# Optimization experiments

Measured on AMD Instinct MI355X. Metric: run time of the kernel, lower is better.

The kernel has to match this reference:

```python
import jax, jax.numpy as jnp
import numpy as np

B, S, D, H = 2, 2048, 1024, 16
HD = D // H  # head_dim = 64


def setup_inputs() -> dict:
    key = jax.random.key(0)
    ks = jax.random.split(key, 9)
    s_in = 1.0 / np.sqrt(D)
    inp = {
        "hidden_state": jax.random.normal(ks[0], (B, S, D), dtype=jnp.float32),
        # per-head projections, stacked: [H, D, HD]
        "Wq": jax.random.uniform(ks[1], (H, D, HD), jnp.float32, -s_in, s_in),
        "bq": jax.random.uniform(ks[2], (H, HD), jnp.float32, -s_in, s_in),
        "Wk": jax.random.uniform(ks[3], (H, D, HD), jnp.float32, -s_in, s_in),
        "bk": jax.random.uniform(ks[4], (H, HD), jnp.float32, -s_in, s_in),
        "Wv": jax.random.uniform(ks[5], (H, D, HD), jnp.float32, -s_in, s_in),
        "bv": jax.random.uniform(ks[6], (H, HD), jnp.float32, -s_in, s_in),
        # output linear: [D, D]
        "Wo": jax.random.uniform(ks[7], (D, D), jnp.float32, -s_in, s_in),
        "bo": jax.random.uniform(ks[8], (D,), jnp.float32, -s_in, s_in),
    }
    return inp


def reference(hidden_state, Wq, bq, Wk, bk, Wv, bv, Wo, bo):
    # fused per-head projections: [B, H, S, HD]
    q = jnp.einsum("bsd,hde->bhse", hidden_state, Wq) + bq[None, :, None, :]
    k = jnp.einsum("bsd,hde->bhse", hidden_state, Wk) + bk[None, :, None, :]
    v = jnp.einsum("bsd,hde->bhse", hidden_state, Wv) + bv[None, :, None, :]
    scale = 1.0 / jnp.sqrt(jnp.float32(HD))
    scores = jnp.einsum("bhse,bhte->bhst", q, k) * scale  # [B, H, S, S]
    weights = jax.nn.softmax(scores, axis=-1)
    ctx = jnp.einsum("bhst,bhte->bhse", weights, v)       # [B, H, S, HD]
    # concat heads along last dim -> [B, S, D]
    ctx = jnp.transpose(ctx, (0, 2, 1, 3)).reshape(B, S, D)
    return ctx @ Wo + bo
```

## Files before the change

kernel.cpp:

```cpp
#include <hip/hip_runtime.h>
#include <hip/hip_bf16.h>
#include <math.h>

#define BB 2
#define SS 2048
#define DD 1024
#define HH 16
#define HD 64

typedef __attribute__((ext_vector_type(8))) _Float16 f16x8;
typedef __attribute__((ext_vector_type(2))) __fp16 fp16x2;
typedef __attribute__((ext_vector_type(8))) unsigned short u16x8;
typedef __attribute__((ext_vector_type(4))) float f32x4;
typedef __attribute__((ext_vector_type(16))) float f32x16;
typedef __attribute__((ext_vector_type(4))) unsigned short u16x4;

__device__ __forceinline__ unsigned short hbits(_Float16 h) {
    union { _Float16 h; unsigned short s; } u; u.h = h; return u.s;
}

__device__ __forceinline__ int swz(int row, int grp) {
    return (row << 6) + (((grp) ^ (row & 7)) << 3);
}

__device__ __forceinline__ float fexp2(float x) {
#if __has_builtin(__builtin_amdgcn_exp2f)
    return __builtin_amdgcn_exp2f(x);
#else
    return exp2f(x);
#endif
}

__device__ __forceinline__ u16x4 pack4(float p0, float p1, float p2, float p3) {
#if __has_builtin(__builtin_amdgcn_cvt_pkrtz)
    union { fp16x2 h[2]; u16x4 u; } pu;
    pu.h[0] = __builtin_amdgcn_cvt_pkrtz(p0, p1);
    pu.h[1] = __builtin_amdgcn_cvt_pkrtz(p2, p3);
    return pu.u;
#else
    u16x4 r;
    r[0] = hbits((_Float16)p0); r[1] = hbits((_Float16)p1);
    r[2] = hbits((_Float16)p2); r[3] = hbits((_Float16)p3);
    return r;
#endif
}

__device__ __forceinline__ void gload_lds16(const unsigned short* g, unsigned short* l) {
#if __has_builtin(__builtin_amdgcn_global_load_lds)
    auto gp = (const __attribute__((address_space(1))) unsigned int*)(uintptr_t)g;
    auto lp = (__attribute__((address_space(3))) unsigned int*)(uintptr_t)l;
    __builtin_amdgcn_global_load_lds(gp, lp, 16, 0, 0);
#else
    *(u16x8*)(l + (threadIdx.x & 63) * 8) = *(const u16x8*)g;
#endif
}

__device__ __forceinline__ void wait4_barrier() {
    asm volatile("s_waitcnt vmcnt(4) lgkmcnt(0)\n\ts_barrier" ::: "memory");
}
__device__ __forceinline__ void wait6_barrier() {
    asm volatile("s_waitcnt vmcnt(6) lgkmcnt(0)\n\ts_barrier" ::: "memory");
}
__device__ __forceinline__ void wait0_barrier() {
    asm volatile("s_waitcnt vmcnt(0) lgkmcnt(0)\n\ts_barrier" ::: "memory");
}

__global__ __launch_bounds__(256) void prep_convert(
    const float* __restrict__ X,
    const float* __restrict__ Wq, const float* __restrict__ Wk,
    const float* __restrict__ Wv, const float* __restrict__ Wo,
    unsigned short* __restrict__ Xh2, unsigned short* __restrict__ WT)
{
    __shared__ __align__(16) unsigned short LT[64 * 68];
    const int bid = blockIdx.x;
    const int tid = threadIdx.x;

    if (bid < 2048) {
        const int mblk = bid >> 4;
        const int kg   = bid & 15;
        {
            const int r  = tid >> 3;
            const int c0 = (tid & 7) * 8;
            const float* src = X + (size_t)(mblk * 32 + r) * DD + kg * 64 + c0;
            float4 a = *(const float4*)src;
            float4 b = *(const float4*)(src + 4);
            unsigned short* d = &LT[r * 68 + c0];
            d[0] = hbits((_Float16)a.x); d[1] = hbits((_Float16)a.y);
            d[2] = hbits((_Float16)a.z); d[3] = hbits((_Float16)a.w);
            d[4] = hbits((_Float16)b.x); d[5] = hbits((_Float16)b.y);
            d[6] = hbits((_Float16)b.z); d[7] = hbits((_Float16)b.w);
        }
        __syncthreads();
        const int fbl = tid >> 6, l = tid & 63;
        const int row = l & 31, c = fbl * 16 + (l >> 5) * 8;
        u16x8 v = *(const u16x8*)&LT[row * 68 + c];
        *(u16x8*)&Xh2[((size_t)mblk * 64 + kg * 4 + fbl) * 512 + l * 8] = v;
        return;
    }

    const int t = bid - 2048;
    if (t < 768) {
        const int nt = t >> 4, ktile = t & 15;
        const int sel = nt >> 4, hh = nt & 15;
        const float* Ws = (sel == 0) ? Wq : ((sel == 1) ? Wk : Wv);
        const float* src = Ws + (size_t)hh * (DD * HD) + (size_t)ktile * 64 * HD;
        const int outRow0 = nt * 64;
        const int kcol0   = ktile * 64;

        const int e = tid & 63, dq = tid >> 6;
#pragma unroll
        for (int p = 0; p < 16; p++) {
            const int dl = p * 4 + dq;
            LT[e * 68 + dl] = hbits((_Float16)src[(size_t)dl * HD + e]);
        }
        __syncthreads();
#pragma unroll
        for (int p = 0; p < 2; p++) {
            const int sidx = p * 2048 + tid * 8;
            const int fb = sidx >> 9;
            const int l  = (sidx >> 3) & 63;
            const int nb = fb >> 2, kb = fb & 3;
            const int ee = nb * 32 + (l & 31);
            const int dl = kb * 16 + (l >> 5) * 8;
            u16x8 v = *(const u16x8*)&LT[ee * 68 + dl];
            *(u16x8*)&WT[(((size_t)(outRow0 >> 5) + nb) * 64 + (kcol0 >> 4) + kb) * 512
                         + l * 8] = v;
        }
    } else {
        const int tt = t - 768;
        const int nt = tt & 15, ktile = tt >> 4;
        const float* src = Wo + (size_t)ktile * 64 * DD + nt * 64;
        const int outRow0 = 3072 + nt * 64;
        const int kcol0 = ktile * 64;

        const int e = tid & 63, dq = tid >> 6;
#pragma unroll
        for (int p = 0; p < 16; p++) {
            const int dl = p * 4 + dq;
            LT[e * 68 + dl] = hbits((_Float16)src[(size_t)dl * DD + e]);
        }
        __syncthreads();
        const int eo = tid >> 2, d16 = (tid & 3) * 16;
#pragma unroll
        for (int j = 0; j < 4; j++) {
            *(ushort4*)&WT[(size_t)(outRow0 + eo) * DD + kcol0 + d16 + j * 4] =
                *(const ushort4*)&LT[eo * 68 + d16 + j * 4];
        }
    }
}

#define GBM 128
#define GBN 128
#define GBK 64
#define NKT (DD / GBK)
#define QBK 32
#define QNKT (DD / QBK)

__global__ __launch_bounds__(256, 3) void qkv_gemm(
    const unsigned short* __restrict__ Xh2, const unsigned short* __restrict__ WT2,
    const float* __restrict__ bq, const float* __restrict__ bk,
    const float* __restrict__ bv,
    unsigned short* __restrict__ qh, unsigned short* __restrict__ kh,
    unsigned short* __restrict__ vTs, unsigned int* __restrict__ kc2)
{
    __shared__ __align__(16) unsigned short As[3][8 * 512];
    __shared__ __align__(16) unsigned short Bs[3][8 * 512];

    const int tid  = threadIdx.x;
    const int m0   = blockIdx.y * GBM;
    const int n0   = blockIdx.x * GBN;
    const int lane = tid & 63;
    const int w    = tid >> 6;
    const int wm   = w & 1, wn = w >> 1;
    const int l31  = lane & 31, h = lane >> 5;

    f32x16 acc[2][2];
#pragma unroll
    for (int i = 0; i < 2; i++)
#pragma unroll
        for (int j = 0; j < 2; j++)
#pragma unroll
            for (int k = 0; k < 16; k++) acc[i][j][k] = 0.f;

    const size_t mb0 = (size_t)(m0 >> 5);
    const size_t nb0 = (size_t)(n0 >> 5);

    auto STAGE = [&](int buf, int t) {
#pragma unroll
        for (int p = 0; p < 4; p++) {
            const int c = p * 4 + w;
            const unsigned short* src;
            unsigned short* dst;
            if (c < 8) {
                src = Xh2 + ((mb0 + (c >> 1)) * 64 + t * 2 + (c & 1)) * 512 + lane * 8;
                dst = &As[buf][c * 512];
            } else {
                const int d = c - 8;
                src = WT2 + ((nb0 + (d >> 1)) * 64 + t * 2 + (d & 1)) * 512 + lane * 8;
                dst = &Bs[buf][d * 512];
            }
            gload_lds16(src, dst);
        }
    };

    STAGE(0, 0);
    STAGE(1, 1);
    wait0_barrier();

    int cur = 0, pre = 2;
    for (int t = 0; t < QNKT; t++) {
        if (t + 2 < QNKT) STAGE(pre, t + 2);
        f16x8 af[2][2], bf[2][2];
#pragma unroll
        for (int mi = 0; mi < 2; mi++)
#pragma unroll
            for (int kb = 0; kb < 2; kb++)
                af[mi][kb] = *(const f16x8*)
                    &As[cur][(((wm * 2 + mi) << 1) + kb) * 512 + lane * 8];
#pragma unroll
        for (int ni = 0; ni < 2; ni++)
#pragma unroll
            for (int kb = 0; kb < 2; kb++)
                bf[ni][kb] = *(const f16x8*)
                    &Bs[cur][(((wn * 2 + ni) << 1) + kb) * 512 + lane * 8];
#pragma unroll
        for (int kb = 0; kb < 2; kb++)
#pragma unroll
            for (int mi = 0; mi < 2; mi++)
#pragma unroll
                for (int ni = 0; ni < 2; ni++)
                    acc[mi][ni] = __builtin_amdgcn_mfma_f32_32x32x16_f16(
                        af[mi][kb], bf[ni][kb], acc[mi][ni], 0, 0, 0);
        if (t < QNKT - 2)       wait4_barrier();
        else if (t == QNKT - 2) wait0_barrier();
        cur = (cur == 2) ? 0 : cur + 1;
        pre = (pre == 2) ? 0 : pre + 1;
    }

    const int sel = n0 >> 10;
    const int hw  = ((n0 + wn * 64) >> 6) & 15;
    const int bblk = m0 >> 11;
    const float* bias = (sel == 0) ? bq : ((sel == 1) ? bk : bv);
    const size_t bh_base = ((size_t)bblk * HH + hw) * (size_t)SS * HD;
    float wmx = 0.0f;
#pragma unroll
    for (int mi = 0; mi < 2; mi++) {
#pragma unroll
        for (int r = 0; r < 16; r++) {
            const int srow = wm * 64 + mi * 32 + (r & 3) + 8 * (r >> 2) + 4 * h;
            const int s = (m0 + srow) & (SS - 1);
            const int s63 = s & 63;
            float v2 = 0.0f;
#pragma unroll
            for (int ni = 0; ni < 2; ni++) {
                const int e = ni * 32 + l31;
                const float val = acc[mi][ni][r] + bias[hw * HD + e];
                if (sel == 0) {
                    qh[bh_base + (size_t)s * HD + e] = hbits((_Float16)val);
                } else if (sel == 1) {
                    v2 = fmaf(val, val, v2);
                    kh[bh_base + (size_t)(s >> 6) * 4096 + swz(s63, e >> 3) + (e & 7)] =
                        hbits((_Float16)val);
                } else {
                    vTs[bh_base + (size_t)(s >> 6) * 4096 + swz(e, s63 >> 3) + (s63 & 7)] =
                        hbits((_Float16)val);
                }
            }
            if (sel == 1) {
                v2 += __shfl_xor(v2, 1);
                v2 += __shfl_xor(v2, 2);
                v2 += __shfl_xor(v2, 4);
                v2 += __shfl_xor(v2, 8);
                v2 += __shfl_xor(v2, 16);
                wmx = fmaxf(wmx, v2);
            }
        }
    }
    if (sel == 1) {
        wmx = fmaxf(wmx, __shfl_xor(wmx, 32));
        if (lane == 0)
            atomicMax(&kc2[bblk * HH + hw], __float_as_uint(wmx));
    }
}

__global__ __launch_bounds__(256, 2) void out_gemm(
    const unsigned short* __restrict__ Ctxh, const unsigned short* __restrict__ WoT,
    const float* __restrict__ bo, float* __restrict__ out)
{
    __shared__ __align__(16) unsigned short As[3][16 * 512];
    __shared__ __align__(16) unsigned short Bs[3][8 * 512];

    const int tid = threadIdx.x;
    const int f  = blockIdx.y * 16 + blockIdx.x;
    const int fs = (f & 7) * 64 + (f >> 3);
    const int bx = fs % 16, by = fs / 16;
    const int m0 = by * 128;
    const int n0 = bx * 64;
    const int lane = tid & 63;
    const int w = tid >> 6;
    const int wm = w & 1, wn = w >> 1;
    const int l15 = lane & 15, quad = lane >> 4;

    int g_off[4];
#pragma unroll
    for (int p = 0; p < 4; p++) {
        const int c = p * 4 + w;
        g_off[p] = ((c >> 1) * 16 + l15) * DD + (c & 1) * 32 + quad * 8;
    }

    f32x4 acc[4][2];
#pragma unroll
    for (int i = 0; i < 4; i++)
#pragma unroll
        for (int j = 0; j < 2; j++) acc[i][j] = (f32x4){0.f, 0.f, 0.f, 0.f};

    const unsigned short* Abase = Ctxh + (size_t)m0 * DD;
    const unsigned short* Bbase = WoT + (size_t)n0 * DD;

#pragma unroll
    for (int p = 0; p < 4; p++)
        gload_lds16(Abase + g_off[p], &As[0][(p * 4 + w) * 512]);
#pragma unroll
    for (int p = 0; p < 2; p++)
        gload_lds16(Bbase + g_off[p], &Bs[0][(p * 4 + w) * 512]);
#pragma unroll
    for (int p = 0; p < 4; p++)
        gload_lds16(Abase + g_off[p] + GBK, &As[1][(p * 4 + w) * 512]);
#pragma unroll
    for (int p = 0; p < 2; p++)
        gload_lds16(Bbase + g_off[p] + GBK, &Bs[1][(p * 4 + w) * 512]);
    wait0_barrier();

    int cur = 0, pre = 2;
    for (int it = 0; it < NKT; it++) {
        if (it + 2 < NKT) {
            const int kt2 = (it + 2) * GBK;
#pragma unroll
            for (int p = 0; p < 4; p++)
                gload_lds16(Abase + g_off[p] + kt2, &As[pre][(p * 4 + w) * 512]);
#pragma unroll
            for (int p = 0; p < 2; p++)
                gload_lds16(Bbase + g_off[p] + kt2, &Bs[pre][(p * 4 + w) * 512]);
        }
#pragma unroll
        for (int ks = 0; ks < 2; ks++) {
            f16x8 af[4], bf[2];
#pragma unroll
            for (int i = 0; i < 4; i++)
                af[i] = *(const f16x8*)&As[cur][((wm * 4 + i) * 2 + ks) * 512 + lane * 8];
#pragma unroll
            for (int j = 0; j < 2; j++)
                bf[j] = *(const f16x8*)&Bs[cur][((wn * 2 + j) * 2 + ks) * 512 + lane * 8];
#pragma unroll
            for (int ns = 0; ns < 2; ns++)
#pragma unroll
                for (int ms = 0; ms < 4; ms++)
                    acc[ms][ns] = __builtin_amdgcn_mfma_f32_16x16x32_f16(
                        af[ms], bf[ns], acc[ms][ns], 0, 0, 0);
        }
        if (it < NKT - 2)       wait6_barrier();
        else if (it == NKT - 2) wait0_barrier();
        cur = (cur == 2) ? 0 : cur + 1;
        pre = (pre == 2) ? 0 : pre + 1;
    }

#pragma unroll
    for (int ms = 0; ms < 4; ms++) {
#pragma unroll
        for (int rr = 0; rr < 4; rr++) {
            const size_t m = (size_t)(m0 + wm * 64 + ms * 16 + quad * 4 + rr);
#pragma unroll
            for (int ns = 0; ns < 2; ns++) {
                const int n = n0 + wn * 32 + ns * 16 + l15;
                out[m * DD + n] = acc[ms][ns][rr] + bo[n];
            }
        }
    }
}

#define TQB 128
#define TKB 64
#define NT (SS / TKB)
#define C1 0.1803368801111204f

__global__ __launch_bounds__(256, 2) void attn_mfma(
    const unsigned short* __restrict__ qh, const unsigned short* __restrict__ kh,
    const unsigned short* __restrict__ vTs, const unsigned int* __restrict__ kc2,
    unsigned short* __restrict__ ctxh)
{
    __shared__ __align__(16) unsigned short KL [3][TKB * 64];
    __shared__ __align__(16) unsigned short VtL[3][HD * 64];
    __shared__ __align__(16) unsigned short PsL[4][32 * 64];

    const int tid  = threadIdx.x;
    const int lane = tid & 63;
    const int w    = tid >> 6;
    const int l15  = lane & 15;
    const int quad = lane >> 4;
    const int f  = blockIdx.y * 16 + blockIdx.x;
    const int fs = (f & 7) * 64 + (f >> 3);
    const int bh = fs >> 4;
    const int q0 = (fs & 15) * TQB;

    const float kfac = sqrtf(__uint_as_float(kc2[bh])) * 1.01f * C1;

    f16x8 qf[2][2];
    float M2[2];
#pragma unroll
    for (int msub = 0; msub < 2; msub++) {
        const unsigned short* qrow =
            qh + ((size_t)bh * SS + q0 + w * 32 + msub * 16 + l15) * HD;
        float nq2 = 0.0f;
#pragma unroll
        for (int dstep = 0; dstep < 2; dstep++) {
            qf[msub][dstep] = *(const f16x8*)&qrow[dstep * 32 + quad * 8];
#pragma unroll
            for (int j = 0; j < 8; j++) {
                const float x = (float)qf[msub][dstep][j];
                nq2 = fmaf(x, x, nq2);
            }
        }
        nq2 += __shfl_xor(nq2, 16);
        nq2 += __shfl_xor(nq2, 32);
        M2[msub] = sqrtf(nq2) * kfac;
    }

    f16x8 ones;
#pragma unroll
    for (int j = 0; j < 8; j++) ones[j] = (_Float16)1.0f;

    f32x4 o[2][4], lones[2];
#pragma unroll
    for (int ms = 0; ms < 2; ms++) {
        lones[ms] = (f32x4){0.f, 0.f, 0.f, 0.f};
#pragma unroll
        for (int e = 0; e < 4; e++) o[ms][e] = (f32x4){0.f, 0.f, 0.f, 0.f};
    }

    const unsigned short* kb0 = kh  + (size_t)bh * SS * HD;
    const unsigned short* vb0 = vTs + (size_t)bh * SS * HD;

    gload_lds16(kb0 + tid * 8,        &KL [0][w * 512]);
    gload_lds16(kb0 + 2048 + tid * 8, &KL [0][2048 + w * 512]);
    gload_lds16(vb0 + tid * 8,        &VtL[0][w * 512]);
    gload_lds16(vb0 + 2048 + tid * 8, &VtL[0][2048 + w * 512]);
    gload_lds16(kb0 + 4096 + tid * 8, &KL [1][w * 512]);
    gload_lds16(kb0 + 6144 + tid * 8, &KL [1][2048 + w * 512]);
    gload_lds16(vb0 + 4096 + tid * 8, &VtL[1][w * 512]);
    gload_lds16(vb0 + 6144 + tid * 8, &VtL[1][2048 + w * 512]);
    wait0_barrier();

    int cur = 0, pre = 2;
    for (int t = 0; t < NT; t++) {
        if (t + 2 < NT) {
            const unsigned short* kb = kb0 + (size_t)(t + 2) * 4096;
            const unsigned short* vb = vb0 + (size_t)(t + 2) * 4096;
            gload_lds16(kb + tid * 8,        &KL [pre][w * 512]);
            gload_lds16(kb + 2048 + tid * 8, &KL [pre][2048 + w * 512]);
            gload_lds16(vb + tid * 8,        &VtL[pre][w * 512]);
            gload_lds16(vb + 2048 + tid * 8, &VtL[pre][2048 + w * 512]);
        }

        f32x4 sc[2][4];
        __builtin_amdgcn_s_setprio(1);
#pragma unroll
        for (int ksub = 0; ksub < 4; ksub++) {
            const int row = ksub * 16 + l15;
            f16x8 k0 = *(const f16x8*)&KL[cur][swz(row, quad)];
            f16x8 k1 = *(const f16x8*)&KL[cur][swz(row, 4 + quad)];
#pragma unroll
            for (int msub = 0; msub < 2; msub++) {
                f32x4 a = (f32x4){0.f, 0.f, 0.f, 0.f};
                a = __builtin_amdgcn_mfma_f32_16x16x32_f16(k0, qf[msub][0], a, 0, 0, 0);
                a = __builtin_amdgcn_mfma_f32_16x16x32_f16(k1, qf[msub][1], a, 0, 0, 0);
                sc[msub][ksub] = a;
            }
        }
        __builtin_amdgcn_s_setprio(0);

#pragma unroll
        for (int msub = 0; msub < 2; msub++) {
            const int prow = msub * 16 + l15;
#pragma unroll
            for (int ksub = 0; ksub < 4; ksub++) {
                const float p0 = fexp2(fmaf(sc[msub][ksub][0], C1, -M2[msub]));
                const float p1 = fexp2(fmaf(sc[msub][ksub][1], C1, -M2[msub]));
                const float p2 = fexp2(fmaf(sc[msub][ksub][2], C1, -M2[msub]));
                const float p3 = fexp2(fmaf(sc[msub][ksub][3], C1, -M2[msub]));
                *(u16x4*)&PsL[w][swz(prow, ksub * 2 + (quad >> 1)) + (quad & 1) * 4] =
                    pack4(p0, p1, p2, p3);
            }
        }

        __builtin_amdgcn_s_setprio(1);
#pragma unroll
        for (int kj = 0; kj < 2; kj++) {
            f16x8 pa[2];
#pragma unroll
            for (int msub = 0; msub < 2; msub++)
                pa[msub] = *(const f16x8*)&PsL[w][swz(msub * 16 + l15, kj * 4 + quad)];
            lones[0] = __builtin_amdgcn_mfma_f32_16x16x32_f16(pa[0], ones, lones[0], 0, 0, 0);
            lones[1] = __builtin_amdgcn_mfma_f32_16x16x32_f16(pa[1], ones, lones[1], 0, 0, 0);
#pragma unroll
            for (int esub = 0; esub < 4; esub++) {
                f16x8 vr = *(const f16x8*)&VtL[cur][swz(esub * 16 + l15, kj * 4 + quad)];
                o[0][esub] = __builtin_amdgcn_mfma_f32_16x16x32_f16(pa[0], vr, o[0][esub], 0, 0, 0);
                o[1][esub] = __builtin_amdgcn_mfma_f32_16x16x32_f16(pa[1], vr, o[1][esub], 0, 0, 0);
            }
        }
        __builtin_amdgcn_s_setprio(0);

        if (t < NT - 2)       wait4_barrier();
        else if (t == NT - 2) wait0_barrier();
        cur = (cur == 2) ? 0 : cur + 1;
        pre = (pre == 2) ? 0 : pre + 1;
    }

    const int b = bh >> 4;
    const int hh = bh & 15;
#pragma unroll
    for (int msub = 0; msub < 2; msub++) {
#pragma unroll
        for (int rr = 0; rr < 4; rr++) {
            const float linv = 1.0f / lones[msub][rr];
            const int row = q0 + w * 32 + msub * 16 + quad * 4 + rr;
#pragma unroll
            for (int esub = 0; esub < 4; esub++) {
                ctxh[((size_t)b * SS + row) * DD + hh * HD + esub * 16 + l15] =
                    hbits((_Float16)(o[msub][esub][rr] * linv));
            }
        }
    }
}

extern "C" void kernel_launch(void* const* d_in, const int* in_sizes, int n_in,
                              void* d_out, int out_size, void* d_ws, size_t ws_size,
                              hipStream_t stream) {
    const float* X  = (const float*)d_in[0];
    const float* Wq = (const float*)d_in[1];
    const float* bq = (const float*)d_in[2];
    const float* Wk = (const float*)d_in[3];
    const float* bk = (const float*)d_in[4];
    const float* Wv = (const float*)d_in[5];
    const float* bv = (const float*)d_in[6];
    const float* Wo = (const float*)d_in[7];
    const float* bo = (const float*)d_in[8];
    float* out = (float*)d_out;

    const size_t NB2 = (size_t)4096 * 1024 * 2;
    unsigned char* w8 = (unsigned char*)d_ws;
    unsigned short* Xh2  = (unsigned short*)(w8);
    unsigned short* WT   = (unsigned short*)(w8 + NB2);
    unsigned short* qh   = (unsigned short*)(w8 + 2 * NB2);
    unsigned short* kh   = (unsigned short*)(w8 + 3 * NB2);
    unsigned short* vTs  = (unsigned short*)(w8 + 4 * NB2);
    unsigned short* ctxh = (unsigned short*)(w8 + 5 * NB2);
    unsigned int*   kc2  = (unsigned int*)(w8 + 6 * NB2);
    unsigned short* WoT  = WT + (size_t)3072 * 1024;

    (void)hipMemsetAsync(kc2, 0, BB * HH * sizeof(unsigned int), stream);

    prep_convert<<<dim3(3072), 256, 0, stream>>>(X, Wq, Wk, Wv, Wo, Xh2, WT);

    qkv_gemm<<<dim3(3072 / GBN, 4096 / GBM), 256, 0, stream>>>(
        Xh2, WT, bq, bk, bv, qh, kh, vTs, kc2);

    attn_mfma<<<dim3(SS / TQB, BB * HH), 256, 0, stream>>>(qh, kh, vTs, kc2, ctxh);

    out_gemm<<<dim3(1024 / 64, 4096 / 128), 256, 0, stream>>>(ctxh, WoT, bo, out);
}
```

Measured before the change: 214.4 us.

## Switch attention to 32x32x16 MFMA tiles with per-lane row-sum accumulation

Rewrites the attention inner loop to use 32x32x16 f16 MFMAs, so each wave handles its 32 query rows as one tile, in place of 16x16x32 MFMAs over two 16-row subtiles. The score layout now gives each lane one query row, so the softmax denominator is summed directly in VALU instead of via an extra MFMA against a ones vector. The output is written as 4-element vector stores. This cuts MFMA instruction count and removes the ones-MFMA overhead, but changes register pressure and LDS access patterns, and the K/V tile is now processed in two 32-key halves.

```diff
diff --git a/kernel.cpp b/kernel.cpp
--- a/kernel.cpp
+++ b/kernel.cpp
@@ -395,8 +395,8 @@
     const int tid  = threadIdx.x;
     const int lane = tid & 63;
     const int w    = tid >> 6;
-    const int l15  = lane & 15;
-    const int quad = lane >> 4;
+    const int l31  = lane & 31;
+    const int h    = lane >> 5;
     const int f  = blockIdx.y * 16 + blockIdx.x;
     const int fs = (f & 7) * 64 + (f >> 3);
     const int bh = fs >> 4;
@@ -404,38 +404,31 @@
 
     const float kfac = sqrtf(__uint_as_float(kc2[bh])) * 1.01f * C1;
 
-    f16x8 qf[2][2];
-    float M2[2];
-#pragma unroll
-    for (int msub = 0; msub < 2; msub++) {
+    f16x8 qf[4];
+    float M2;
+    {
         const unsigned short* qrow =
-            qh + ((size_t)bh * SS + q0 + w * 32 + msub * 16 + l15) * HD;
+            qh + ((size_t)bh * SS + q0 + w * 32 + l31) * HD;
         float nq2 = 0.0f;
 #pragma unroll
-        for (int dstep = 0; dstep < 2; dstep++) {
-            qf[msub][dstep] = *(const f16x8*)&qrow[dstep * 32 + quad * 8];
+        for (int kf = 0; kf < 4; kf++) {
+            qf[kf] = *(const f16x8*)&qrow[kf * 16 + h * 8];
 #pragma unroll
             for (int j = 0; j < 8; j++) {
-                const float x = (float)qf[msub][dstep][j];
+                const float x = (float)qf[kf][j];
                 nq2 = fmaf(x, x, nq2);
             }
         }
-        nq2 += __shfl_xor(nq2, 16);
         nq2 += __shfl_xor(nq2, 32);
-        M2[msub] = sqrtf(nq2) * kfac;
-    }
-
-    f16x8 ones;
-#pragma unroll
-    for (int j = 0; j < 8; j++) ones[j] = (_Float16)1.0f;
-
-    f32x4 o[2][4], lones[2];
-#pragma unroll
-    for (int ms = 0; ms < 2; ms++) {
-        lones[ms] = (f32x4){0.f, 0.f, 0.f, 0.f};
-#pragma unroll
-        for (int e = 0; e < 4; e++) o[ms][e] = (f32x4){0.f, 0.f, 0.f, 0.f};
-    }
+        M2 = sqrtf(nq2) * kfac;
+    }
+
+    f32x16 o[2];
+#pragma unroll
+    for (int eb = 0; eb < 2; eb++)
+#pragma unroll
+        for (int r = 0; r < 16; r++) o[eb][r] = 0.f;
+    float lsum = 0.0f;
 
     const unsigned short* kb0 = kh  + (size_t)bh * SS * HD;
     const unsigned short* vb0 = vTs + (size_t)bh * SS * HD;
@@ -461,54 +454,49 @@
             gload_lds16(vb + 2048 + tid * 8, &VtL[pre][2048 + w * 512]);
         }
 
-        f32x4 sc[2][4];
-        __builtin_amdgcn_s_setprio(1);
-#pragma unroll
-        for (int ksub = 0; ksub < 4; ksub++) {
-            const int row = ksub * 16 + l15;
-            f16x8 k0 = *(const f16x8*)&KL[cur][swz(row, quad)];
-            f16x8 k1 = *(const f16x8*)&KL[cur][swz(row, 4 + quad)];
-#pragma unroll
-            for (int msub = 0; msub < 2; msub++) {
-                f32x4 a = (f32x4){0.f, 0.f, 0.f, 0.f};
-                a = __builtin_amdgcn_mfma_f32_16x16x32_f16(k0, qf[msub][0], a, 0, 0, 0);
-                a = __builtin_amdgcn_mfma_f32_16x16x32_f16(k1, qf[msub][1], a, 0, 0, 0);
-                sc[msub][ksub] = a;
-            }
-        }
-        __builtin_amdgcn_s_setprio(0);
-
-#pragma unroll
-        for (int msub = 0; msub < 2; msub++) {
-            const int prow = msub * 16 + l15;
-#pragma unroll
-            for (int ksub = 0; ksub < 4; ksub++) {
-                const float p0 = fexp2(fmaf(sc[msub][ksub][0], C1, -M2[msub]));
-                const float p1 = fexp2(fmaf(sc[msub][ksub][1], C1, -M2[msub]));
-                const float p2 = fexp2(fmaf(sc[msub][ksub][2], C1, -M2[msub]));
-                const float p3 = fexp2(fmaf(sc[msub][ksub][3], C1, -M2[msub]));
-                *(u16x4*)&PsL[w][swz(prow, ksub * 2 + (quad >> 1)) + (quad & 1) * 4] =
-                    pack4(p0, p1, p2, p3);
-            }
-        }
-
-        __builtin_amdgcn_s_setprio(1);
-#pragma unroll
-        for (int kj = 0; kj < 2; kj++) {
-            f16x8 pa[2];
-#pragma unroll
-            for (int msub = 0; msub < 2; msub++)
-                pa[msub] = *(const f16x8*)&PsL[w][swz(msub * 16 + l15, kj * 4 + quad)];
-            lones[0] = __builtin_amdgcn_mfma_f32_16x16x32_f16(pa[0], ones, lones[0], 0, 0, 0);
-            lones[1] = __builtin_amdgcn_mfma_f32_16x16x32_f16(pa[1], ones, lones[1], 0, 0, 0);
-#pragma unroll
-            for (int esub = 0; esub < 4; esub++) {
-                f16x8 vr = *(const f16x8*)&VtL[cur][swz(esub * 16 + l15, kj * 4 + quad)];
-                o[0][esub] = __builtin_amdgcn_mfma_f32_16x16x32_f16(pa[0], vr, o[0][esub], 0, 0, 0);
-                o[1][esub] = __builtin_amdgcn_mfma_f32_16x16x32_f16(pa[1], vr, o[1][esub], 0, 0, 0);
-            }
-        }
-        __builtin_amdgcn_s_setprio(0);
+#pragma unroll
+        for (int kb = 0; kb < 2; kb++) {
+            f32x16 sc;
+#pragma unroll
+            for (int r = 0; r < 16; r++) sc[r] = 0.f;
+            __builtin_amdgcn_s_setprio(1);
+#pragma unroll
+            for (int kf = 0; kf < 4; kf++) {
+                const int gd = kf * 2 + h;
+                f16x8 kfr = *(const f16x8*)
+                    &KL[cur][(kb * 32 + l31) * 64 + ((gd ^ (l31 & 7)) << 3)];
+                sc = __builtin_amdgcn_mfma_f32_32x32x16_f16(kfr, qf[kf], sc, 0, 0, 0);
+            }
+            __builtin_amdgcn_s_setprio(0);
+
+            float p[16];
+#pragma unroll
+            for (int r = 0; r < 16; r++) {
+                p[r] = fexp2(fmaf(sc[r], C1, -M2));
+                lsum += p[r];
+            }
+#pragma unroll
+            for (int j = 0; j < 4; j++) {
+                const int g = kb * 4 + j;
+                *(u16x4*)&PsL[w][l31 * 64 + ((g ^ (l31 & 7)) << 3) + h * 4] =
+                    pack4(p[4 * j], p[4 * j + 1], p[4 * j + 2], p[4 * j + 3]);
+            }
+
+            __builtin_amdgcn_s_setprio(1);
+#pragma unroll
+            for (int kf = 0; kf < 2; kf++) {
+                const int gg = kb * 4 + kf * 2 + h;
+                f16x8 pb = *(const f16x8*)
+                    &PsL[w][l31 * 64 + ((gg ^ (l31 & 7)) << 3)];
+#pragma unroll
+                for (int eb = 0; eb < 2; eb++) {
+                    f16x8 va = *(const f16x8*)
+                        &VtL[cur][(eb * 32 + l31) * 64 + ((gg ^ (l31 & 7)) << 3)];
+                    o[eb] = __builtin_amdgcn_mfma_f32_32x32x16_f16(va, pb, o[eb], 0, 0, 0);
+                }
+            }
+            __builtin_amdgcn_s_setprio(0);
+        }
 
         if (t < NT - 2)       wait4_barrier();
         else if (t == NT - 2) wait0_barrier();
@@ -516,19 +504,21 @@
         pre = (pre == 2) ? 0 : pre + 1;
     }
 
-    const int b = bh >> 4;
+    lsum += __shfl_xor(lsum, 32);
+    const float linv = 1.0f / lsum;
+    const int b  = bh >> 4;
     const int hh = bh & 15;
-#pragma unroll
-    for (int msub = 0; msub < 2; msub++) {
-#pragma unroll
-        for (int rr = 0; rr < 4; rr++) {
-            const float linv = 1.0f / lones[msub][rr];
-            const int row = q0 + w * 32 + msub * 16 + quad * 4 + rr;
-#pragma unroll
-            for (int esub = 0; esub < 4; esub++) {
-                ctxh[((size_t)b * SS + row) * DD + hh * HD + esub * 16 + l15] =
-                    hbits((_Float16)(o[msub][esub][rr] * linv));
-            }
+    const size_t rowbase = ((size_t)b * SS + q0 + w * 32 + l31) * DD + hh * HD;
+#pragma unroll
+    for (int eb = 0; eb < 2; eb++) {
+#pragma unroll
+        for (int jj = 0; jj < 4; jj++) {
+            u16x4 oc;
+#pragma unroll
+            for (int i = 0; i < 4; i++)
+                oc[i] = hbits((_Float16)(o[eb][4 * jj + i] * linv));
+            const int e0 = eb * 32 + 8 * jj + 4 * h;
+            *(u16x4*)&ctxh[rowbase + e0] = oc;
         }
     }
 }
```

After: 220.7 us. 3.0% more time.

## Double the attention query tile and compute softmax exponentials inline

Applied to the files above, without the earlier changes.

Doubles the attention query tile from 128 to 256 rows per block, so each wave handles 64 query rows. Each staged K/V tile is then reused across twice as many queries, which halves the global K/V traffic. The exp2/pack of scores is moved into the QK MFMA loop, removing the separate score array and pass. In exchange the grid shrinks to 256 blocks with launch bounds of one block per CU, so latency hiding drops and register pressure per thread rises.

```diff
diff --git a/kernel.cpp b/kernel.cpp
--- a/kernel.cpp
+++ b/kernel.cpp
@@ -378,38 +378,38 @@
     }
 }
 
-#define TQB 128
+#define TQB 256
 #define TKB 64
 #define NT (SS / TKB)
 #define C1 0.1803368801111204f
 
-__global__ __launch_bounds__(256, 2) void attn_mfma(
+__global__ __launch_bounds__(256, 1) void attn_mfma(
     const unsigned short* __restrict__ qh, const unsigned short* __restrict__ kh,
     const unsigned short* __restrict__ vTs, const unsigned int* __restrict__ kc2,
     unsigned short* __restrict__ ctxh)
 {
     __shared__ __align__(16) unsigned short KL [3][TKB * 64];
     __shared__ __align__(16) unsigned short VtL[3][HD * 64];
-    __shared__ __align__(16) unsigned short PsL[4][32 * 64];
+    __shared__ __align__(16) unsigned short PsL[4][64 * 64];
 
     const int tid  = threadIdx.x;
     const int lane = tid & 63;
     const int w    = tid >> 6;
     const int l15  = lane & 15;
     const int quad = lane >> 4;
-    const int f  = blockIdx.y * 16 + blockIdx.x;
-    const int fs = (f & 7) * 64 + (f >> 3);
-    const int bh = fs >> 4;
-    const int q0 = (fs & 15) * TQB;
+    const int f  = blockIdx.y * 8 + blockIdx.x;
+    const int fs = (f & 7) * 32 + (f >> 3);
+    const int bh = fs >> 3;
+    const int q0 = (fs & 7) * TQB;
 
     const float kfac = sqrtf(__uint_as_float(kc2[bh])) * 1.01f * C1;
 
-    f16x8 qf[2][2];
-    float M2[2];
-#pragma unroll
-    for (int msub = 0; msub < 2; msub++) {
+    f16x8 qf[4][2];
+    float M2[4];
+#pragma unroll
+    for (int msub = 0; msub < 4; msub++) {
         const unsigned short* qrow =
-            qh + ((size_t)bh * SS + q0 + w * 32 + msub * 16 + l15) * HD;
+            qh + ((size_t)bh * SS + q0 + w * 64 + msub * 16 + l15) * HD;
         float nq2 = 0.0f;
 #pragma unroll
         for (int dstep = 0; dstep < 2; dstep++) {
@@ -429,9 +429,9 @@
 #pragma unroll
     for (int j = 0; j < 8; j++) ones[j] = (_Float16)1.0f;
 
-    f32x4 o[2][4], lones[2];
-#pragma unroll
-    for (int ms = 0; ms < 2; ms++) {
+    f32x4 o[4][4], lones[4];
+#pragma unroll
+    for (int ms = 0; ms < 4; ms++) {
         lones[ms] = (f32x4){0.f, 0.f, 0.f, 0.f};
 #pragma unroll
         for (int e = 0; e < 4; e++) o[ms][e] = (f32x4){0.f, 0.f, 0.f, 0.f};
@@ -440,28 +440,23 @@
     const unsigned short* kb0 = kh  + (size_t)bh * SS * HD;
     const unsigned short* vb0 = vTs + (size_t)bh * SS * HD;
 
-    gload_lds16(kb0 + tid * 8,        &KL [0][w * 512]);
-    gload_lds16(kb0 + 2048 + tid * 8, &KL [0][2048 + w * 512]);
-    gload_lds16(vb0 + tid * 8,        &VtL[0][w * 512]);
-    gload_lds16(vb0 + 2048 + tid * 8, &VtL[0][2048 + w * 512]);
-    gload_lds16(kb0 + 4096 + tid * 8, &KL [1][w * 512]);
-    gload_lds16(kb0 + 6144 + tid * 8, &KL [1][2048 + w * 512]);
-    gload_lds16(vb0 + 4096 + tid * 8, &VtL[1][w * 512]);
-    gload_lds16(vb0 + 6144 + tid * 8, &VtL[1][2048 + w * 512]);
+    auto STAGE = [&](int buf, int t) {
+        const unsigned short* kb = kb0 + (size_t)t * 4096;
+        const unsigned short* vb = vb0 + (size_t)t * 4096;
+        gload_lds16(kb + tid * 8,        &KL [buf][w * 512]);
+        gload_lds16(kb + 2048 + tid * 8, &KL [buf][2048 + w * 512]);
+        gload_lds16(vb + tid * 8,        &VtL[buf][w * 512]);
+        gload_lds16(vb + 2048 + tid * 8, &VtL[buf][2048 + w * 512]);
+    };
+
+    STAGE(0, 0);
+    STAGE(1, 1);
     wait0_barrier();
 
     int cur = 0, pre = 2;
     for (int t = 0; t < NT; t++) {
-        if (t + 2 < NT) {
-            const unsigned short* kb = kb0 + (size_t)(t + 2) * 4096;
-            const unsigned short* vb = vb0 + (size_t)(t + 2) * 4096;
-            gload_lds16(kb + tid * 8,        &KL [pre][w * 512]);
-            gload_lds16(kb + 2048 + tid * 8, &KL [pre][2048 + w * 512]);
-            gload_lds16(vb + tid * 8,        &VtL[pre][w * 512]);
-            gload_lds16(vb + 2048 + tid * 8, &VtL[pre][2048 + w * 512]);
-        }
-
-        f32x4 sc[2][4];
+        if (t + 2 < NT) STAGE(pre, t + 2);
+
         __builtin_amdgcn_s_setprio(1);
 #pragma unroll
         for (int ksub = 0; ksub < 4; ksub++) {
@@ -469,43 +464,37 @@
             f16x8 k0 = *(const f16x8*)&KL[cur][swz(row, quad)];
             f16x8 k1 = *(const f16x8*)&KL[cur][swz(row, 4 + quad)];
 #pragma unroll
-            for (int msub = 0; msub < 2; msub++) {
+            for (int msub = 0; msub < 4; msub++) {
                 f32x4 a = (f32x4){0.f, 0.f, 0.f, 0.f};
                 a = __builtin_amdgcn_mfma_f32_16x16x32_f16(k0, qf[msub][0], a, 0, 0, 0);
                 a = __builtin_amdgcn_mfma_f32_16x16x32_f16(k1, qf[msub][1], a, 0, 0, 0);
-                sc[msub][ksub] = a;
+                const float p0 = fexp2(fmaf(a[0], C1, -M2[msub]));
+                const float p1 = fexp2(fmaf(a[1], C1, -M2[msub]));
+                const float p2 = fexp2(fmaf(a[2], C1, -M2[msub]));
+                const float p3 = fexp2(fmaf(a[3], C1, -M2[msub]));
+                *(u16x4*)&PsL[w][swz(msub * 16 + l15, ksub * 2 + (quad >> 1))
+                                 + (quad & 1) * 4] = pack4(p0, p1, p2, p3);
             }
         }
         __builtin_amdgcn_s_setprio(0);
 
-#pragma unroll
-        for (int msub = 0; msub < 2; msub++) {
-            const int prow = msub * 16 + l15;
-#pragma unroll
-            for (int ksub = 0; ksub < 4; ksub++) {
-                const float p0 = fexp2(fmaf(sc[msub][ksub][0], C1, -M2[msub]));
-                const float p1 = fexp2(fmaf(sc[msub][ksub][1], C1, -M2[msub]));
-                const float p2 = fexp2(fmaf(sc[msub][ksub][2], C1, -M2[msub]));
-                const float p3 = fexp2(fmaf(sc[msub][ksub][3], C1, -M2[msub]));
-                *(u16x4*)&PsL[w][swz(prow, ksub * 2 + (quad >> 1)) + (quad & 1) * 4] =
-                    pack4(p0, p1, p2, p3);
-            }
-        }
-
         __builtin_amdgcn_s_setprio(1);
 #pragma unroll
         for (int kj = 0; kj < 2; kj++) {
-            f16x8 pa[2];
-#pragma unroll
-            for (int msub = 0; msub < 2; msub++)
+            f16x8 pa[4];
+#pragma unroll
+            for (int msub = 0; msub < 4; msub++) {
                 pa[msub] = *(const f16x8*)&PsL[w][swz(msub * 16 + l15, kj * 4 + quad)];
-            lones[0] = __builtin_amdgcn_mfma_f32_16x16x32_f16(pa[0], ones, lones[0], 0, 0, 0);
-            lones[1] = __builtin_amdgcn_mfma_f32_16x16x32_f16(pa[1], ones, lones[1], 0, 0, 0);
+                lones[msub] = __builtin_amdgcn_mfma_f32_16x16x32_f16(
+                    pa[msub], ones, lones[msub], 0, 0, 0);
+            }
 #pragma unroll
             for (int esub = 0; esub < 4; esub++) {
                 f16x8 vr = *(const f16x8*)&VtL[cur][swz(esub * 16 + l15, kj * 4 + quad)];
-                o[0][esub] = __builtin_amdgcn_mfma_f32_16x16x32_f16(pa[0], vr, o[0][esub], 0, 0, 0);
-                o[1][esub] = __builtin_amdgcn_mfma_f32_16x16x32_f16(pa[1], vr, o[1][esub], 0, 0, 0);
+#pragma unroll
+                for (int msub = 0; msub < 4; msub++)
+                    o[msub][esub] = __builtin_amdgcn_mfma_f32_16x16x32_f16(
+                        pa[msub], vr, o[msub][esub], 0, 0, 0);
             }
         }
         __builtin_amdgcn_s_setprio(0);
@@ -516,14 +505,14 @@
         pre = (pre == 2) ? 0 : pre + 1;
     }
 
-    const int b = bh >> 4;
+    const int b  = bh >> 4;
     const int hh = bh & 15;
 #pragma unroll
-    for (int msub = 0; msub < 2; msub++) {
+    for (int msub = 0; msub < 4; msub++) {
 #pragma unroll
         for (int rr = 0; rr < 4; rr++) {
             const float linv = 1.0f / lones[msub][rr];
-            const int row = q0 + w * 32 + msub * 16 + quad * 4 + rr;
+            const int row = q0 + w * 64 + msub * 16 + quad * 4 + rr;
 #pragma unroll
             for (int esub = 0; esub < 4; esub++) {
                 ctxh[((size_t)b * SS + row) * DD + hh * HD + esub * 16 + l15] =
```

After: 219.8 us. +2.5%, slower.
